# Kernel tuning notes

Measured on AMD Instinct MI355X. Metric: run time of the kernel, lower is better.

## Reference

```python
import jax, jax.numpy as jnp
import numpy as np

B, SL = 16, 512
S = SL - 1            # context length after shift (length=1)
E = 256               # embedding_size / hidden_size
NH = 4                # num_heads
K = 4                 # conv1d_kernel_size
I = 2 * E             # mLSTM inner dim (_inner_embedding_dim = 2*E)
DHM = I // NH         # mLSTM head dim
DHS = E // NH         # sLSTM head dim
NB, BS = I // 4, 4    # qkv_proj_blocksize=4 block-diagonal projections
F = 384               # gated FFN up dim = round_up(1.3*256, 64)
NUM_SKILLS, NUM_Q = 500, 10000
EPS = 1e-5


def _ln(x, w):
    mu = x.mean(-1, keepdims=True)
    var = x.var(-1, keepdims=True)
    return (x - mu) / jnp.sqrt(var + EPS) * w


def _causal_dwconv(x, w, b):
    # x: (B,S,C), depthwise causal conv with kernel (C,K)
    xt = jnp.transpose(x, (0, 2, 1))
    y = jax.lax.conv_general_dilated(
        xt, w[:, None, :], (1,), [(K - 1, 0)],
        dimension_numbers=('NCH', 'OIH', 'NCH'),
        feature_group_count=x.shape[-1])
    return jnp.transpose(y, (0, 2, 1)) + b


def _headwise(x, w):
    # block-diagonal linear: w (NB, BS, BS)
    xb = x.reshape(x.shape[0], x.shape[1], NB, BS)
    return jnp.einsum('bsnd,nod->bsno', xb, w).reshape(x.shape)


def _forward(questions, responses, skills,
             q_embed, qa_embed, q_embed_diff, qa_embed_diff, difficult_param,
             ln0_w, m_up_w, m_up_b, m_conv_w, m_conv_b, m_q_w, m_k_w, m_v_w,
             m_ig_w, m_ig_b, m_fg_w, m_fg_b, m_outnorm_w, m_skip, m_down_w, m_down_b,
             ln1_w, s_conv_w, s_conv_b, s_gate_w, s_rec_w, s_bias, s_gn_w,
             ln2_w, ffn_up_w, ffn_up_b, ffn_down_w, ffn_down_b,
             postnorm_w, out_w1, out_b1, out_w2, out_b2, out_w3, out_b3):
    pid = questions[:, :-1]
    q_data = skills[:, :-1]
    q_shft = skills[:, 1:]
    target = (responses * (responses > -1).astype(responses.dtype))[:, :-1]

    q_e = q_embed[q_data]                              # (B,S,E)
    qa_e = qa_embed[target] + q_e
    pid_e = difficult_param[pid]                       # (B,S,1)
    q_e = q_e + pid_e * q_embed_diff[q_data]
    qa_e = qa_e + pid_e * qa_embed_diff[target]

    # ---- xLSTM stack: block 0 = mLSTM block, block 1 = sLSTM block + gated FFN ----
    x = qa_e  # dropout is identity in eval

    # mLSTM block: x = x + mlstm_layer(LN(x))
    h = _ln(x, ln0_w)
    up = h @ m_up_w.T + m_up_b                         # (B,S,2I)
    x_m, z = jnp.split(up, 2, axis=-1)
    xc = jax.nn.silu(_causal_dwconv(x_m, m_conv_w, m_conv_b))
    q = _headwise(xc, m_q_w)
    k = _headwise(xc, m_k_w)
    v = _headwise(x_m, m_v_w)
    ifin = jnp.concatenate([q, k, v], axis=-1)         # (B,S,3I)
    ig = jnp.einsum('bsf,hf->bhs', ifin, m_ig_w) + m_ig_b[None, :, None]
    fg = jnp.einsum('bsf,hf->bhs', ifin, m_fg_w) + m_fg_b[None, :, None]
    qh = q.reshape(B, S, NH, DHM).transpose(0, 2, 1, 3)
    kh = k.reshape(B, S, NH, DHM).transpose(0, 2, 1, 3)
    vh = v.reshape(B, S, NH, DHM).transpose(0, 2, 1, 3)
    # parallel stabilized mLSTM
    logf = jax.nn.log_sigmoid(fg)                      # (B,NH,S)
    cs = jnp.concatenate([jnp.zeros((B, NH, 1), logf.dtype), jnp.cumsum(logf, -1)], -1)
    dmat = cs[:, :, 1:, None] - cs[:, :, None, 1:]     # (B,NH,S,S): sum of logf over (s,t]
    ltr = jnp.tril(jnp.ones((S, S), bool))
    logD = jnp.where(ltr, dmat, -jnp.inf) + ig[:, :, None, :]
    maxD = jnp.max(logD, -1, keepdims=True)
    D = jnp.exp(logD - maxD)
    qk = jnp.einsum('bhtd,bhsd->bhts', qh, kh) * (DHM ** -0.5)
    C = qk * D
    norm = jnp.maximum(jnp.abs(C.sum(-1, keepdims=True)), jnp.exp(-maxD))
    hh = jnp.einsum('bhts,bhsd->bhtd', C / (norm + 1e-6), vh)
    # multi-head layernorm (per head over DHM), weight on flattened dim
    hn = (hh - hh.mean(-1, keepdims=True)) / jnp.sqrt(hh.var(-1, keepdims=True) + EPS)
    hflat = hn.transpose(0, 2, 1, 3).reshape(B, S, I) * m_outnorm_w
    hout = (hflat + m_skip * xc) * jax.nn.silu(z)
    x = x + (hout @ m_down_w.T + m_down_b)

    # sLSTM block: x = x + slstm_layer(LN(x)); x = x + ffn(LN(x))
    h = _ln(x, ln1_w)
    hc = jax.nn.silu(_causal_dwconv(h, s_conv_w, s_conv_b))
    hh4 = h.reshape(B, S, NH, DHS)
    hc4 = hc.reshape(B, S, NH, DHS)
    gi = jnp.einsum('bsnd,nod->bsno', hc4, s_gate_w[0])   # i,f from conv path
    gf = jnp.einsum('bsnd,nod->bsno', hc4, s_gate_w[1])
    gz = jnp.einsum('bsnd,nod->bsno', hh4, s_gate_w[2])   # z,o from x path
    go = jnp.einsum('bsnd,nod->bsno', hh4, s_gate_w[3])
    wx = jnp.stack([gi, gf, gz, go], axis=2) + s_bias[None, None]  # (B,S,4,NH,DHS)

    def step(carry, wx_t):
        y, c, n, m = carry
        raw = wx_t + jnp.einsum('bnd,gnde->bgne', y, s_rec_w)
        iraw, fraw, zraw, oraw = raw[:, 0], raw[:, 1], raw[:, 2], raw[:, 3]
        logfplusm = m + jax.nn.log_sigmoid(fraw)
        mnew = jnp.maximum(iraw, logfplusm)
        ig_ = jnp.exp(iraw - mnew)
        fg_ = jnp.exp(logfplusm - mnew)
        cnew = fg_ * c + ig_ * jnp.tanh(zraw)
        nnew = fg_ * n + ig_
        ynew = jax.nn.sigmoid(oraw) * cnew / nnew
        return (ynew, cnew, nnew, mnew), ynew

    z0 = jnp.zeros((B, NH, DHS), x.dtype)
    _, ys = jax.lax.scan(step, (z0, z0, z0, z0), jnp.swapaxes(wx, 0, 1))
    y = jnp.swapaxes(ys, 0, 1)                           # (B,S,NH,DHS)
    yn = (y - y.mean(-1, keepdims=True)) / jnp.sqrt(y.var(-1, keepdims=True) + EPS)
    x = x + yn.reshape(B, S, E) * s_gn_w

    # gated FFN (relu)
    h = _ln(x, ln2_w)
    gate, upf = jnp.split(h @ ffn_up_w.T + ffn_up_b, 2, axis=-1)
    x = x + (jax.nn.relu(gate) * upf) @ ffn_down_w.T + ffn_down_b

    d = _ln(x, postnorm_w)                               # post_blocks_norm

    fam = jnp.where((target == 1)[..., None], d, 0.0)
    unfam = jnp.where((target == 0)[..., None], d, 0.0)
    d2 = d - pid_e
    cq = jnp.concatenate([d2, q_e, fam, unfam], axis=-1)  # (B,S,4E)
    o = jax.nn.relu(cq @ out_w1.T + out_b1)
    o = jax.nn.relu(o @ out_w2.T + out_b2)
    probs = jax.nn.sigmoid(o @ out_w3.T + out_b3)
    pred = jnp.take_along_axis(probs, q_shft[..., None], axis=-1)[..., 0]
    return pred                                          # (B,S)


def setup_inputs():
    key = jax.random.key(0)
    ks = iter(jax.random.split(key, 64))
    def rn(shape, s=0.02):
        return jax.random.normal(next(ks), shape, jnp.float32) * s
    return dict(
        questions=jax.random.randint(next(ks), (B, SL), 0, NUM_Q),
        responses=jax.random.randint(next(ks), (B, SL), 0, 2),
        skills=jax.random.randint(next(ks), (B, SL), 0, NUM_SKILLS),
        attention_mask=jnp.ones((B, SL), jnp.int32),
        q_embed=rn((NUM_SKILLS, E), 1.0),
        qa_embed=rn((2, E), 1.0),
        q_embed_diff=rn((NUM_SKILLS + 1, E), 1.0),
        qa_embed_diff=rn((2 * NUM_SKILLS + 1, E), 1.0),
        difficult_param=rn((NUM_Q + 1, 1), 0.1),
        ln0_w=jnp.ones((E,)),
        m_up_w=rn((2 * I, E)), m_up_b=jnp.zeros((2 * I,)),
        m_conv_w=rn((I, K), 0.1), m_conv_b=jnp.zeros((I,)),
        m_q_w=rn((NB, BS, BS), 0.1), m_k_w=rn((NB, BS, BS), 0.1), m_v_w=rn((NB, BS, BS), 0.1),
        m_ig_w=rn((NH, 3 * I)), m_ig_b=jnp.zeros((NH,)),
        m_fg_w=rn((NH, 3 * I)), m_fg_b=jnp.zeros((NH,)),
        m_outnorm_w=jnp.ones((I,)), m_skip=jnp.ones((I,)),
        m_down_w=rn((E, I)), m_down_b=jnp.zeros((E,)),
        ln1_w=jnp.ones((E,)),
        s_conv_w=rn((E, K), 0.1), s_conv_b=jnp.zeros((E,)),
        s_gate_w=rn((4, NH, DHS, DHS), 0.1),
        s_rec_w=rn((4, NH, DHS, DHS), 0.05),
        s_bias=jnp.zeros((4, NH, DHS)),
        s_gn_w=jnp.ones((E,)),
        ln2_w=jnp.ones((E,)),
        ffn_up_w=rn((2 * F, E)), ffn_up_b=jnp.zeros((2 * F,)),
        ffn_down_w=rn((E, F)), ffn_down_b=jnp.zeros((E,)),
        postnorm_w=jnp.ones((E,)),
        out_w1=rn((2 * E, 4 * E)), out_b1=jnp.zeros((2 * E,)),
        out_w2=rn((E, 2 * E)), out_b2=jnp.zeros((E,)),
        out_w3=rn((NUM_SKILLS, E)), out_b3=jnp.zeros((NUM_SKILLS,)),
    )


def reference(questions, responses, skills, attention_mask,
              q_embed, qa_embed, q_embed_diff, qa_embed_diff, difficult_param,
              ln0_w, m_up_w, m_up_b, m_conv_w, m_conv_b, m_q_w, m_k_w, m_v_w,
              m_ig_w, m_ig_b, m_fg_w, m_fg_b, m_outnorm_w, m_skip, m_down_w, m_down_b,
              ln1_w, s_conv_w, s_conv_b, s_gate_w, s_rec_w, s_bias, s_gn_w,
              ln2_w, ffn_up_w, ffn_up_b, ffn_down_w, ffn_down_b,
              postnorm_w, out_w1, out_b1, out_w2, out_b2, out_w3, out_b3):
    return _forward(questions, responses, skills,
                    q_embed, qa_embed, q_embed_diff, qa_embed_diff, difficult_param,
                    ln0_w, m_up_w, m_up_b, m_conv_w, m_conv_b, m_q_w, m_k_w, m_v_w,
                    m_ig_w, m_ig_b, m_fg_w, m_fg_b, m_outnorm_w, m_skip, m_down_w, m_down_b,
                    ln1_w, s_conv_w, s_conv_b, s_gate_w, s_rec_w, s_bias, s_gn_w,
                    ln2_w, ffn_up_w, ffn_up_b, ffn_down_w, ffn_down_b,
                    postnorm_w, out_w1, out_b1, out_w2, out_b2, out_w3, out_b3)
```

## Files before the change

kernel.cpp:

```cpp
#include <hip/hip_runtime.h>
#include <hip/hip_bf16.h>

#define B_    16
#define SL_   512
#define S_    511
#define E_    256
#define NH_   4
#define I_    512
#define DHM_  128
#define DHS_  64
#define F_    384
#define NP_   8192
#define NROW  (B_*S_)
#define EPS_  1e-5f

typedef __hip_bfloat16 bf16;
typedef unsigned short u16;
typedef __bf16 bf16x8v __attribute__((ext_vector_type(8)));
typedef float  f32x4v  __attribute__((ext_vector_type(4)));

__device__ __forceinline__ float rcp_(float x){ return __builtin_amdgcn_rcpf(x); }
__device__ __forceinline__ float sig_(float x){ return rcp_(1.f+__expf(-x)); }
__device__ __forceinline__ float silu_(float x){ return x*sig_(x); }
__device__ __forceinline__ float logsig_(float x){ return fminf(x,0.f) - __logf(1.f + __expf(-fabsf(x))); }
__device__ __forceinline__ float expneg_(float x){ return __expf(fminf(x,0.f)); }
__device__ __forceinline__ float expclamp_(float x){ return __expf(fminf(fmaxf(x,-80.f),80.f)); }
__device__ __forceinline__ float tanh_(float x){ return 1.f - 2.f*rcp_(__expf(2.f*x)+1.f); }

__global__ __launch_bounds__(256) void k_cvt16(const float* __restrict__ src, bf16* __restrict__ dst, int n){
  int i=blockIdx.x*256+threadIdx.x;
  if(i<n) dst[i]=__float2bfloat16(src[i]);
}
__global__ __launch_bounds__(256) void k_cvt16i(const float* __restrict__ src, bf16* __restrict__ dst){
  int i=blockIdx.x*256+threadIdx.x;
  int rp=i>>8, c=i&255;
  int j=rp>>1, p=rp&1;
  dst[i]=__float2bfloat16(src[(size_t)(j + p*F_)*E_ + c]);
}
__global__ __launch_bounds__(256) void k_cvtsplit(const float* __restrict__ src,
  bf16* __restrict__ hi, bf16* __restrict__ lo, int n){
  int i=blockIdx.x*256+threadIdx.x;
  if(i<n){
    float v=src[i];
    bf16 h=__float2bfloat16(v);
    hi[i]=h;
    lo[i]=__float2bfloat16(v-__bfloat162float(h));
  }
}
__global__ __launch_bounds__(256) void k_wtrans(const float* __restrict__ src, float* __restrict__ dst){
  int i = blockIdx.x*256+threadIdx.x;
  int blk = i>>12;
  int d = (i>>6)&63;
  int e = i&63;
  dst[(size_t)(blk*64+d)*64+e] = src[(size_t)(blk*64+e)*64+d];
}

__global__ __launch_bounds__(256) void k_wfrag(const float* __restrict__ rw, bf16* __restrict__ wf){
  int i = blockIdx.x*256+threadIdx.x;
  int j  = i&7;
  int l  = (i>>3)&63;
  int kf = (i>>9)&1;
  int t  = (i>>10)&15;
  int n  = i>>14;
  int g = t>>2;
  int e = (t&3)*16 + (l&15);
  int d = (l>>4)*16 + kf*8 + j;
  wf[i] = __float2bfloat16(rw[((size_t)((g*4+n)*64 + d))*64 + e]);
}

__global__ __launch_bounds__(256) void k_embed(
  const int* __restrict__ questions, const int* __restrict__ responses, const int* __restrict__ skills,
  const float* __restrict__ q_embed, const float* __restrict__ qa_embed,
  const float* __restrict__ q_embed_diff, const float* __restrict__ qa_embed_diff,
  const float* __restrict__ difficult_param, const float* __restrict__ ln0w,
  float* __restrict__ x, float* __restrict__ qe,
  bf16* __restrict__ h_hi, bf16* __restrict__ h_lo,
  float* __restrict__ pide, int* __restrict__ tgt, int* __restrict__ qsh)
{
  __shared__ float red[256];
  int r = blockIdx.x; int e = threadIdx.x;
  float xa = 0.f;
  if (r < NROW){
    int b = r / S_, s = r % S_;
    int pid  = questions[b*SL_+s];
    int qd   = skills[b*SL_+s];
    int resp = responses[b*SL_+s];
    int t    = (resp > -1) ? resp : 0;
    float pe = difficult_param[pid];
    float q0 = q_embed[qd*E_+e];
    xa = q0 + qa_embed[t*E_+e] + pe*qa_embed_diff[t*E_+e];
    float qn = q0 + pe*q_embed_diff[qd*E_+e];
    x[(size_t)r*E_+e]=xa; qe[(size_t)r*E_+e]=qn;
    if (e==0){ pide[r]=pe; tgt[r]=t; qsh[r]=skills[b*SL_+s+1]; }
  } else {
    x[(size_t)r*E_+e]=0.f; qe[(size_t)r*E_+e]=0.f;
    if (e==0){ pide[r]=0.f; tgt[r]=-7; qsh[r]=0; }
  }
  red[e]=xa; __syncthreads();
  for(int s2=128;s2>0;s2>>=1){ if(e<s2) red[e]+=red[e+s2]; __syncthreads(); }
  float mu = red[0]*(1.f/E_); __syncthreads();
  float d = xa-mu;
  red[e]=d*d; __syncthreads();
  for(int s2=128;s2>0;s2>>=1){ if(e<s2) red[e]+=red[e+s2]; __syncthreads(); }
  float var = red[0]*(1.f/E_);
  float o = d*rsqrtf(var+EPS_)*ln0w[e];
  bf16 hv = __float2bfloat16(o);
  h_hi[(size_t)r*E_+e] = hv;
  h_lo[(size_t)r*E_+e] = __float2bfloat16(o-__bfloat162float(hv));
}

__global__ __launch_bounds__(256) void k_ln(
  const float* __restrict__ in, const float* __restrict__ w, float* __restrict__ out)
{
  __shared__ float red[256];
  int r = blockIdx.x, t = threadIdx.x;
  float v = in[(size_t)r*E_+t];
  red[t]=v; __syncthreads();
  for(int s=128;s>0;s>>=1){ if(t<s) red[t]+=red[t+s]; __syncthreads(); }
  float mu = red[0]*(1.f/E_); __syncthreads();
  float d = v-mu;
  red[t]=d*d; __syncthreads();
  for(int s=128;s>0;s>>=1){ if(t<s) red[t]+=red[t+s]; __syncthreads(); }
  float var = red[0]*(1.f/E_);
  out[(size_t)r*E_+t] = d*rsqrtf(var+EPS_)*w[t];
}

__global__ __launch_bounds__(256) void k_gemm16s(
  const bf16* __restrict__ Ah, const bf16* __restrict__ Al,
  const bf16* __restrict__ Bh, const bf16* __restrict__ Bl,
  const float* __restrict__ bias, float* __restrict__ C, int M, int K)
{
  int tid=threadIdx.x;
  int wave=tid>>6, lane=tid&63;
  int wr=wave>>1, wc=wave&1;
  int row0=blockIdx.y*64 + wr*32;
  int col0=blockIdx.x*64 + wc*32;
  int lrow = lane&15, lq = lane>>4;
  f32x4v acc[2][2] = {};
  size_t aoff = (size_t)(row0+lrow)*K + lq*8;
  size_t boff = (size_t)(col0+lrow)*K + lq*8;
  for(int k0=0;k0<K;k0+=32){
    bf16x8v ah0=*(const bf16x8v*)(Ah+aoff+k0), ah1=*(const bf16x8v*)(Ah+aoff+(size_t)16*K+k0);
    bf16x8v al0=*(const bf16x8v*)(Al+aoff+k0), al1=*(const bf16x8v*)(Al+aoff+(size_t)16*K+k0);
    bf16x8v bh0=*(const bf16x8v*)(Bh+boff+k0), bh1=*(const bf16x8v*)(Bh+boff+(size_t)16*K+k0);
    bf16x8v bl0=*(const bf16x8v*)(Bl+boff+k0), bl1=*(const bf16x8v*)(Bl+boff+(size_t)16*K+k0);
    acc[0][0]=__builtin_amdgcn_mfma_f32_16x16x32_bf16(ah0,bh0,acc[0][0],0,0,0);
    acc[0][1]=__builtin_amdgcn_mfma_f32_16x16x32_bf16(ah0,bh1,acc[0][1],0,0,0);
    acc[1][0]=__builtin_amdgcn_mfma_f32_16x16x32_bf16(ah1,bh0,acc[1][0],0,0,0);
    acc[1][1]=__builtin_amdgcn_mfma_f32_16x16x32_bf16(ah1,bh1,acc[1][1],0,0,0);
    acc[0][0]=__builtin_amdgcn_mfma_f32_16x16x32_bf16(ah0,bl0,acc[0][0],0,0,0);
    acc[0][1]=__builtin_amdgcn_mfma_f32_16x16x32_bf16(ah0,bl1,acc[0][1],0,0,0);
    acc[1][0]=__builtin_amdgcn_mfma_f32_16x16x32_bf16(ah1,bl0,acc[1][0],0,0,0);
    acc[1][1]=__builtin_amdgcn_mfma_f32_16x16x32_bf16(ah1,bl1,acc[1][1],0,0,0);
    acc[0][0]=__builtin_amdgcn_mfma_f32_16x16x32_bf16(al0,bh0,acc[0][0],0,0,0);
    acc[0][1]=__builtin_amdgcn_mfma_f32_16x16x32_bf16(al0,bh1,acc[0][1],0,0,0);
    acc[1][0]=__builtin_amdgcn_mfma_f32_16x16x32_bf16(al1,bh0,acc[1][0],0,0,0);
    acc[1][1]=__builtin_amdgcn_mfma_f32_16x16x32_bf16(al1,bh1,acc[1][1],0,0,0);
  }
  #pragma unroll
  for(int mi=0;mi<2;mi++){
    #pragma unroll
    for(int ni=0;ni<2;ni++){
      #pragma unroll
      for(int r=0;r<4;r++){
        int row=row0+mi*16+lq*4+r;
        int col=col0+ni*16+lrow;
        C[(size_t)row*M+col]=acc[mi][ni][r] + bias[col];
      }
    }
  }
}

__global__ __launch_bounds__(256) void k_gemm16(
  const bf16* __restrict__ A, const bf16* __restrict__ Bw,
  const float* __restrict__ bias, const float* __restrict__ resid,
  float* __restrict__ C, bf16* __restrict__ C16,
  int M, int K, int relu)
{
  int tid=threadIdx.x;
  int wave=tid>>6, lane=tid&63;
  int wr=wave>>1, wc=wave&1;
  int row0=blockIdx.y*64 + wr*32;
  int col0=blockIdx.x*64 + wc*32;
  int lrow = lane&15, lq = lane>>4;
  f32x4v acc[2][2] = {};
  const bf16* Abase = A  + (size_t)(row0+lrow)*K + lq*8;
  const bf16* Bbase = Bw + (size_t)(col0+lrow)*K + lq*8;
  for(int k0=0;k0<K;k0+=32){
    bf16x8v a0 = *(const bf16x8v*)(Abase + k0);
    bf16x8v a1 = *(const bf16x8v*)(Abase + (size_t)16*K + k0);
    bf16x8v b0 = *(const bf16x8v*)(Bbase + k0);
    bf16x8v b1 = *(const bf16x8v*)(Bbase + (size_t)16*K + k0);
    acc[0][0]=__builtin_amdgcn_mfma_f32_16x16x32_bf16(a0,b0,acc[0][0],0,0,0);
    acc[0][1]=__builtin_amdgcn_mfma_f32_16x16x32_bf16(a0,b1,acc[0][1],0,0,0);
    acc[1][0]=__builtin_amdgcn_mfma_f32_16x16x32_bf16(a1,b0,acc[1][0],0,0,0);
    acc[1][1]=__builtin_amdgcn_mfma_f32_16x16x32_bf16(a1,b1,acc[1][1],0,0,0);
  }
  #pragma unroll
  for(int mi=0;mi<2;mi++){
    #pragma unroll
    for(int ni=0;ni<2;ni++){
      #pragma unroll
      for(int r=0;r<4;r++){
        int row=row0+mi*16+lq*4+r;
        int col=col0+ni*16+lrow;
        float v=acc[mi][ni][r] + (bias? bias[col]:0.f);
        if(relu) v=fmaxf(v,0.f);
        if(resid) v += resid[(size_t)row*M+col];
        if(C)   C[(size_t)row*M+col]=v;
        if(C16) C16[(size_t)row*M+col]=__float2bfloat16(v);
      }
    }
  }
}

__global__ __launch_bounds__(256) void k_gemm16f(
  const bf16* __restrict__ A, const bf16* __restrict__ Bw,
  const float* __restrict__ bias, bf16* __restrict__ out, int K)
{
  int tid=threadIdx.x;
  int wave=tid>>6, lane=tid&63;
  int wr=wave>>1, wc=wave&1;
  int row0=blockIdx.y*64 + wr*32;
  int col0=blockIdx.x*64 + wc*32;
  int lrow = lane&15, lq = lane>>4;
  f32x4v acc[2][2] = {};
  const bf16* Abase = A  + (size_t)(row0+lrow)*K + lq*8;
  const bf16* Bbase = Bw + (size_t)(col0+lrow)*K + lq*8;
  for(int k0=0;k0<K;k0+=32){
    bf16x8v a0 = *(const bf16x8v*)(Abase + k0);
    bf16x8v a1 = *(const bf16x8v*)(Abase + (size_t)16*K + k0);
    bf16x8v b0 = *(const bf16x8v*)(Bbase + k0);
    bf16x8v b1 = *(const bf16x8v*)(Bbase + (size_t)16*K + k0);
    acc[0][0]=__builtin_amdgcn_mfma_f32_16x16x32_bf16(a0,b0,acc[0][0],0,0,0);
    acc[0][1]=__builtin_amdgcn_mfma_f32_16x16x32_bf16(a0,b1,acc[0][1],0,0,0);
    acc[1][0]=__builtin_amdgcn_mfma_f32_16x16x32_bf16(a1,b0,acc[1][0],0,0,0);
    acc[1][1]=__builtin_amdgcn_mfma_f32_16x16x32_bf16(a1,b1,acc[1][1],0,0,0);
  }
  #pragma unroll
  for(int mi=0;mi<2;mi++){
    #pragma unroll
    for(int ni=0;ni<2;ni++){
      #pragma unroll
      for(int r=0;r<4;r++){
        int row=row0+mi*16+lq*4+r;
        int col=col0+ni*16+lrow;
        float v=acc[mi][ni][r] + bias[(col>>1) + (col&1)*F_];
        float o = __shfl_xor(v, 1, 64);
        if(!(lrow&1)){
          out[(size_t)row*F_ + (col>>1)] = __float2bfloat16(fmaxf(v,0.f)*o);
        }
      }
    }
  }
}

__global__ __launch_bounds__(256) void k_conv_silu(
  const float* __restrict__ in, int ild, const float* __restrict__ w, const float* __restrict__ bws,
  float* __restrict__ out, int old_, int C)
{
  int i = blockIdx.x*256 + threadIdx.x;
  int r = i / C, c = i % C;
  if (r >= NP_) return;
  float acc = 0.f;
  if (r < NROW) {
    int b=r/S_, s=r%S_;
    acc = bws[c];
    #pragma unroll
    for(int j=0;j<4;j++){
      int ss=s-3+j;
      if(ss>=0) acc += w[c*4+j] * in[(size_t)(b*S_+ss)*ild + c];
    }
    acc = silu_(acc);
  }
  out[(size_t)r*old_ + c] = acc;
}

__global__ __launch_bounds__(256) void k_headwise(
  const float* __restrict__ xc, const float* __restrict__ xm, int xmld,
  const float* __restrict__ wq, const float* __restrict__ wk, const float* __restrict__ wv,
  bf16* __restrict__ qhi, bf16* __restrict__ qlo,
  bf16* __restrict__ khi, bf16* __restrict__ klo,
  bf16* __restrict__ vhi, bf16* __restrict__ vlo)
{
  int i=blockIdx.x*256+threadIdx.x;
  int r=i/I_, c=i%I_;
  if(r>=NP_) return;
  size_t oi=(size_t)r*I_+c;
  if(r>=NROW){
    bf16 z=__float2bfloat16(0.f);
    qhi[oi]=z; qlo[oi]=z; khi[oi]=z; klo[oi]=z; vhi[oi]=z; vlo[oi]=z;
    return;
  }
  int n=c>>2, o=c&3;
  const float* xcr = xc + (size_t)r*I_ + n*4;
  const float* xmr = xm + (size_t)r*xmld + n*4;
  float aq=0.f, ak=0.f, av=0.f;
  #pragma unroll
  for(int d=0;d<4;d++){
    float xcv=xcr[d], xmv=xmr[d];
    aq += xcv*wq[(n*4+o)*4+d];
    ak += xcv*wk[(n*4+o)*4+d];
    av += xmv*wv[(n*4+o)*4+d];
  }
  bf16 qh=__float2bfloat16(aq); qhi[oi]=qh; qlo[oi]=__float2bfloat16(aq-__bfloat162float(qh));
  bf16 kh=__float2bfloat16(ak); khi[oi]=kh; klo[oi]=__float2bfloat16(ak-__bfloat162float(kh));
  bf16 vh=__float2bfloat16(av); vhi[oi]=vh; vlo[oi]=__float2bfloat16(av-__bfloat162float(vh));
}

__global__ __launch_bounds__(256) void k_igfg(
  const bf16* __restrict__ qhi, const bf16* __restrict__ qlo,
  const bf16* __restrict__ khi, const bf16* __restrict__ klo,
  const bf16* __restrict__ vhi, const bf16* __restrict__ vlo,
  const float* __restrict__ wig, const float* __restrict__ big,
  const float* __restrict__ wfg, const float* __restrict__ bfg,
  float* __restrict__ igb, float* __restrict__ fgb)
{
  int r=blockIdx.x;
  int h=threadIdx.x>>6, lane=threadIdx.x&63;
  int b=r/S_, s=r%S_;
  float acc_i=0.f, acc_f=0.f;
  for(int f=lane; f<1536; f+=64){
    float val;
    if (f<512)       val = __bfloat162float(qhi[(size_t)r*512+f])      + __bfloat162float(qlo[(size_t)r*512+f]);
    else if (f<1024) val = __bfloat162float(khi[(size_t)r*512+f-512])  + __bfloat162float(klo[(size_t)r*512+f-512]);
    else             val = __bfloat162float(vhi[(size_t)r*512+f-1024]) + __bfloat162float(vlo[(size_t)r*512+f-1024]);
    acc_i += val*wig[h*1536+f];
    acc_f += val*wfg[h*1536+f];
  }
  for(int m=32;m;m>>=1){ acc_i+=__shfl_xor(acc_i,m,64); acc_f+=__shfl_xor(acc_f,m,64); }
  if(lane==0){
    igb[(b*4+h)*512+s]=acc_i+big[h];
    fgb[(b*4+h)*512+s]=acc_f+bfg[h];
  }
}

__global__ __launch_bounds__(256) void k_decay(
  const float* __restrict__ igb, const float* __restrict__ fgb,
  float* __restrict__ cs1, float* __restrict__ g, float* __restrict__ M)
{
  int bh = blockIdx.x; int tid = threadIdx.x;
  __shared__ float buf[512];
  __shared__ float buf2[512];
  for (int s=tid; s<512; s+=256)
    buf[s] = (s<S_) ? logsig_(fgb[bh*512+s]) : 0.f;
  __syncthreads();
  for (int off=1; off<512; off<<=1){
    int s0=tid, s1=tid+256;
    float v0 = buf[s0] + ((s0>=off)? buf[s0-off] : 0.f);
    float v1 = buf[s1] + ((s1>=off)? buf[s1-off] : 0.f);
    __syncthreads();
    buf[s0]=v0; buf[s1]=v1;
    __syncthreads();
  }
  for (int s=tid; s<512; s+=256){
    float c = buf[s];
    if (s<S_){
      cs1[bh*512+s]=c;
      float gv = igb[bh*512+s]-c;
      g[bh*512+s]=gv;
      buf2[s]=gv;
    } else buf2[s] = -3.4e38f;
  }
  __syncthreads();
  for (int off=1; off<512; off<<=1){
    int s0=tid, s1=tid+256;
    float v0 = fmaxf(buf2[s0], (s0>=off)? buf2[s0-off] : -3.4e38f);
    float v1 = fmaxf(buf2[s1], (s1>=off)? buf2[s1-off] : -3.4e38f);
    __syncthreads();
    buf2[s0]=v0; buf2[s1]=v1;
    __syncthreads();
  }
  for (int s=tid; s<S_; s+=256) M[bh*512+s] = buf2[s];
}

#define TQ 32
#define TS 32
__global__ __launch_bounds__(256) void k_attn(
  const bf16* __restrict__ qhi, const bf16* __restrict__ qlo,
  const bf16* __restrict__ khi, const bf16* __restrict__ klo,
  const bf16* __restrict__ vhi, const bf16* __restrict__ vlo,
  const float* __restrict__ cs1, const float* __restrict__ g, const float* __restrict__ M,
  const float* __restrict__ onw, const float* __restrict__ skip,
  const float* __restrict__ xc, const float* __restrict__ zA,
  bf16* __restrict__ out16)
{
  __shared__ __align__(16) u16 vThi[128][40];
  __shared__ __align__(16) u16 vTlo[128][40];
  __shared__ __align__(16) u16 phi[32][40];
  __shared__ __align__(16) u16 plo[32][40];
  __shared__ float MtS[32], cssS[32], normS[32], muS[32], rsS[32];
  __shared__ float lsumW[2][32], sumA[2][32], sumB[2][32];

  int tq = blockIdx.x, bh = blockIdx.y;
  int b = bh>>2, h = bh&3;
  int tid = threadIdx.x;
  int wv = tid>>6;
  int tw = wv&1, sw = wv>>1;
  int l = tid&63;
  int lr = l&15, lg = l>>4;
  int t0 = tq*TQ;
  const float sc = 0.08838834764831843f;

  if (tid < 32){
    int t = t0 + tid; int tc = (t<S_)? t : (S_-1);
    MtS[tid]  = M[bh*512 + tc];
    cssS[tid] = cs1[bh*512 + tc];
  }

  bf16x8v qh[4], ql[4];
  {
    size_t qoff = ((size_t)(b*S_ + t0 + tw*16 + lr))*512 + h*128 + lg*8;
    #pragma unroll
    for(int k0=0;k0<4;k0++){
      qh[k0] = *(const bf16x8v*)(qhi + qoff + k0*32);
      ql[k0] = *(const bf16x8v*)(qlo + qoff + k0*32);
    }
  }

  f32x4v accpv[4] = {};
  float lsum[4] = {0.f,0.f,0.f,0.f};

  int t1 = min(t0+TQ, S_);
  int sp = tid>>4, dl = tid&15;

  __syncthreads();

  for (int s0=0; s0<t1; s0+=TS){
    bf16x8v kh[4], kl2[4];
    {
      size_t koff = ((size_t)(b*S_ + s0 + sw*16 + lr))*512 + h*128 + lg*8;
      #pragma unroll
      for(int k0=0;k0<4;k0++){
        kh[k0]  = *(const bf16x8v*)(khi + koff + k0*32);
        kl2[k0] = *(const bf16x8v*)(klo + koff + k0*32);
      }
    }
    u16 vha[8], vhb[8], vla[8], vlb[8];
    {
      const u16* ha = (const u16*)vhi + ((size_t)(b*S_ + s0 + 2*sp))*512 + h*128 + dl;
      const u16* la = (const u16*)vlo + ((size_t)(b*S_ + s0 + 2*sp))*512 + h*128 + dl;
      #pragma unroll
      for(int j=0;j<8;j++){
        vha[j]=ha[16*j]; vhb[j]=ha[512+16*j];
        vla[j]=la[16*j]; vlb[j]=la[512+16*j];
      }
    }
    float g_s = g[bh*512 + s0 + sw*16 + lr];

    f32x4v cqk = {0.f,0.f,0.f,0.f};
    #pragma unroll
    for(int k0=0;k0<4;k0++){
      cqk = __builtin_amdgcn_mfma_f32_16x16x32_bf16(qh[k0], kh[k0],  cqk, 0,0,0);
      cqk = __builtin_amdgcn_mfma_f32_16x16x32_bf16(qh[k0], kl2[k0], cqk, 0,0,0);
      cqk = __builtin_amdgcn_mfma_f32_16x16x32_bf16(ql[k0], kh[k0],  cqk, 0,0,0);
    }

    int s_g = s0 + sw*16 + lr;
    u16 pw_h[4], pw_l[4];
    #pragma unroll
    for(int r=0;r<4;r++){
      int tl = tw*16 + lg*4 + r;
      int t_row = t0 + tl;
      float wvv = ((s_g <= t_row) && (t_row < S_)) ? cqk[r]*sc*expneg_(g_s - MtS[tl]) : 0.f;
      lsum[r] += wvv;
      bf16 hh = __float2bfloat16(wvv);
      float hf = __bfloat162float(hh);
      bf16 ll = __float2bfloat16(wvv - hf);
      __builtin_memcpy(&pw_h[r], &hh, 2);
      __builtin_memcpy(&pw_l[r], &ll, 2);
    }

    __syncthreads();

    #pragma unroll
    for(int r=0;r<4;r++){
      int tl = tw*16 + lg*4 + r;
      phi[tl][sw*16 + lr] = pw_h[r];
      plo[tl][sw*16 + lr] = pw_l[r];
    }
    {
      unsigned* vh32 = (unsigned*)&vThi[0][0];
      unsigned* vl32 = (unsigned*)&vTlo[0][0];
      #pragma unroll
      for(int j=0;j<8;j++){
        int d = dl + 16*j;
        vh32[d*20 + sp] = (unsigned)vha[j] | ((unsigned)vhb[j]<<16);
        vl32[d*20 + sp] = (unsigned)vla[j] | ((unsigned)vlb[j]<<16);
      }
    }

    __syncthreads();

    bf16x8v pah = *(const bf16x8v*)((const void*)(&phi[tw*16 + lr][0] + lg*8));
    bf16x8v pal = *(const bf16x8v*)((const void*)(&plo[tw*16 + lr][0] + lg*8));
    #pragma unroll
    for(int fd=0; fd<4; fd++){
      bf16x8v vbh = *(const bf16x8v*)((const void*)(&vThi[sw*64 + fd*16 + lr][0] + lg*8));
      bf16x8v vbl = *(const bf16x8v*)((const void*)(&vTlo[sw*64 + fd*16 + lr][0] + lg*8));
      accpv[fd] = __builtin_amdgcn_mfma_f32_16x16x32_bf16(pah, vbh, accpv[fd], 0,0,0);
      accpv[fd] = __builtin_amdgcn_mfma_f32_16x16x32_bf16(pah, vbl, accpv[fd], 0,0,0);
      accpv[fd] = __builtin_amdgcn_mfma_f32_16x16x32_bf16(pal, vbh, accpv[fd], 0,0,0);
    }
  }

  #pragma unroll
  for(int r=0;r<4;r++){
    #pragma unroll
    for(int m=1;m<16;m<<=1) lsum[r] += __shfl_xor(lsum[r], m, 16);
  }
  if (lr==0){
    #pragma unroll
    for(int r=0;r<4;r++) lsumW[sw][tw*16 + lg*4 + r] = lsum[r];
  }
  __syncthreads();
  if (tid < 32){
    float ls = lsumW[0][tid] + lsumW[1][tid];
    float maxD = cssS[tid] + MtS[tid];
    float nrm = fmaxf(fabsf(ls), expclamp_(-maxD));
    normS[tid] = rcp_(nrm + 1e-6f);
  }
  __syncthreads();

  float o_[4][4];
  float srow[4]={0.f,0.f,0.f,0.f}, sq[4]={0.f,0.f,0.f,0.f};
  #pragma unroll
  for(int r=0;r<4;r++){
    float scl = normS[tw*16 + lg*4 + r];
    #pragma unroll
    for(int fd=0;fd<4;fd++){
      float o = accpv[fd][r]*scl;
      o_[fd][r] = o;
      srow[r] += o; sq[r] += o*o;
    }
  }
  #pragma unroll
  for(int r=0;r<4;r++){
    #pragma unroll
    for(int m=1;m<16;m<<=1){ srow[r]+=__shfl_xor(srow[r],m,16); sq[r]+=__shfl_xor(sq[r],m,16); }
  }
  if (lr==0){
    #pragma unroll
    for(int r=0;r<4;r++){ sumA[sw][tw*16+lg*4+r]=srow[r]; sumB[sw][tw*16+lg*4+r]=sq[r]; }
  }
  __syncthreads();
  if (tid < 32){
    float mu = (sumA[0][tid]+sumA[1][tid])*(1.f/128.f);
    float ex2= (sumB[0][tid]+sumB[1][tid])*(1.f/128.f);
    muS[tid]=mu;
    rsS[tid]=rsqrtf(fmaxf(ex2 - mu*mu, 0.f)+EPS_);
  }
  __syncthreads();

  #pragma unroll
  for(int fd=0; fd<4; fd++){
    int d = sw*64 + fd*16 + lr;
    float ow = onw[h*128 + d];
    float sk = skip[h*128 + d];
    #pragma unroll
    for(int r=0;r<4;r++){
      int tl = tw*16 + lg*4 + r;
      int t = t0 + tl;
      if (t < S_){
        size_t row = (size_t)(b*S_+t);
        float hf = (o_[fd][r]-muS[tl])*rsS[tl]*ow;
        float xcv = xc[row*512 + h*128 + d];
        float zv  = zA[row*1024 + 512 + h*128 + d];
        out16[row*512 + h*128 + d] = __float2bfloat16((hf + sk*xcv)*silu_(zv));
      }
    }
  }
}

#define WXR 64
__global__ __launch_bounds__(256,2) void k_wx(
  const float* __restrict__ h, const float* __restrict__ hc,
  const float* __restrict__ gwT, const float* __restrict__ gb,
  float* __restrict__ wx)
{
  int rt = blockIdx.x, g = blockIdx.y;
  int tid = threadIdx.x;
  int n = tid>>6, e = tid&63;
  const float* src = (g<2)? hc : h;
  __shared__ __align__(16) float hs[WXR][260];
  float W[64];
  #pragma unroll
  for(int d=0;d<64;d++) W[d] = gwT[(size_t)(((g*4+n)*64+d))*64 + e];
  float bias = gb[(g*4+n)*64+e];
  int row0 = rt*WXR;
  for(int idx=tid; idx<WXR*64; idx+=256){
    int rr = idx>>6, cc4 = (idx&63)*4;
    *(float4*)&hs[rr][cc4] = *(const float4*)(src + (size_t)(row0+rr)*256 + cc4);
  }
  __syncthreads();
  #pragma unroll 4
  for(int rr=0; rr<WXR; ++rr){
    int r = row0+rr;
    if (r>=NROW) break;
    const float* hrow = &hs[rr][n*64];
    float a0=0,a1=0,a2=0,a3=0;
    #pragma unroll
    for(int d=0;d<64;d+=4){
      float4 hv = *(const float4*)&hrow[d];
      a0+=hv.x*W[d]; a1+=hv.y*W[d+1]; a2+=hv.z*W[d+2]; a3+=hv.w*W[d+3];
    }
    int b=r/S_, s=r%S_;
    wx[(((size_t)(b*4+n)*512 + s)*256) + e*4 + g] = bias + ((a0+a1)+(a2+a3));
  }
}

__global__ __launch_bounds__(256,1) void k_scan(
  const float* __restrict__ wx, const bf16* __restrict__ wf, float* __restrict__ y_out)
{
  int bn = blockIdx.x; int b = bn>>2, n = bn&3;
  int tid = threadIdx.x;
  int w = tid>>6;
  int l = tid&63;
  int q = l>>4;
  int el = l&15;
  int e  = w*16 + el;

  __shared__ __align__(16) unsigned short ybuf[2][64];

  if (tid < 128) ((unsigned short*)ybuf)[tid] = 0;
  __syncthreads();

  bf16x8v Wf2[4][2];
  #pragma unroll
  for(int g=0; g<4; ++g){
    #pragma unroll
    for(int kf=0; kf<2; ++kf){
      Wf2[g][kf] = *(const bf16x8v*)(wf + ((size_t)((n*16 + (4*g+w))*2 + kf)*64 + l)*8);
    }
  }

  const float* wxBase = wx + ((size_t)bn*512)*256 + e*4;
  float* yst = y_out + (size_t)(b*S_)*256 + n*64 + e;

  float4 p0,p1,p2,p3;
  p0 = *(const float4*)(wxBase + (size_t)0*256);
  p1 = *(const float4*)(wxBase + (size_t)1*256);
  p2 = *(const float4*)(wxBase + (size_t)2*256);
  p3 = *(const float4*)(wxBase + (size_t)3*256);

  f32x4v z4 = {0.f,0.f,0.f,0.f};
  float c=0.f, nn=0.f, pm=1.f;

  for (int s=0; s<S_; ++s){
    int p = s&1;
    bf16x8v a0 = *(const bf16x8v*)&ybuf[p][16*q];
    bf16x8v a1 = *(const bf16x8v*)&ybuf[p][16*q+8];

    f32x4v acc0,acc1,acc2,acc3, accb0,accb1,accb2,accb3;
    acc0  = __builtin_amdgcn_mfma_f32_16x16x32_bf16(a0, Wf2[0][0], z4, 0,0,0);
    acc1  = __builtin_amdgcn_mfma_f32_16x16x32_bf16(a0, Wf2[1][0], z4, 0,0,0);
    acc2  = __builtin_amdgcn_mfma_f32_16x16x32_bf16(a0, Wf2[2][0], z4, 0,0,0);
    acc3  = __builtin_amdgcn_mfma_f32_16x16x32_bf16(a0, Wf2[3][0], z4, 0,0,0);
    accb0 = __builtin_amdgcn_mfma_f32_16x16x32_bf16(a1, Wf2[0][1], z4, 0,0,0);
    accb1 = __builtin_amdgcn_mfma_f32_16x16x32_bf16(a1, Wf2[1][1], z4, 0,0,0);
    accb2 = __builtin_amdgcn_mfma_f32_16x16x32_bf16(a1, Wf2[2][1], z4, 0,0,0);
    accb3 = __builtin_amdgcn_mfma_f32_16x16x32_bf16(a1, Wf2[3][1], z4, 0,0,0);

    float4 wg = p0; p0=p1; p1=p2; p2=p3;
    { int sp = s+4; if (sp>510) sp=510;
      p3 = *(const float4*)(wxBase + (size_t)sp*256); }

    float iraw=acc0[0]+accb0[0]+wg.x, fraw=acc1[0]+accb1[0]+wg.y;
    float zraw=acc2[0]+accb2[0]+wg.z, oraw=acc3[0]+accb3[0]+wg.w;

    float pe  = __expf(fminf(iraw, 80.f));
    float ef  = __expf(-fraw);
    float e2z = __expf(2.f*zraw);
    float eo  = __expf(-oraw);
    float sf  = rcp_(1.f+ef);
    float ps  = pm*sf;
    float pn  = fmaxf(fmaxf(pe, ps), 1e-30f);
    float rpn = rcp_(pn);
    float fg  = ps*rpn;
    float ig  = pe*rpn;
    float th  = 1.f - 2.f*rcp_(e2z+1.f);
    c  = fg*c + ig*th;
    nn = fmaxf(fg*nn + ig, 1e-30f);
    float y = rcp_(1.f+eo) * c * rcp_(nn);
    pm = pn;

    bf16 hb = __float2bfloat16(y);
    unsigned short hbits; __builtin_memcpy(&hbits,&hb,2);
    if (l < 16){
      ybuf[p^1][e] = hbits;
      yst[(size_t)s*256] = y;
    }
    asm volatile("s_waitcnt lgkmcnt(0)" ::: "memory");
    __builtin_amdgcn_s_barrier();
    asm volatile("" ::: "memory");
    __builtin_amdgcn_sched_barrier(0);
  }
}

__global__ __launch_bounds__(256) void k_ynadd_ln2(
  const float* __restrict__ y, const float* __restrict__ gn,
  float* __restrict__ x, const float* __restrict__ ln2w, bf16* __restrict__ h16)
{
  __shared__ float red[256];
  int r=blockIdx.x, t=threadIdx.x;
  float xv = x[(size_t)r*256+t];
  if (r < NROW){
    float v=y[(size_t)r*256+t];
    float s=v;
    for(int m=32;m;m>>=1) s+=__shfl_xor(s,m,64);
    float mu=s*(1.f/64.f);
    float d=v-mu;
    float q=d*d;
    for(int m=32;m;m>>=1) q+=__shfl_xor(q,m,64);
    float var=q*(1.f/64.f);
    xv += d*rsqrtf(var+EPS_)*gn[t];
    x[(size_t)r*256+t]=xv;
  }
  red[t]=xv; __syncthreads();
  for(int s=128;s>0;s>>=1){ if(t<s) red[t]+=red[t+s]; __syncthreads(); }
  float mu2=red[0]*(1.f/E_); __syncthreads();
  float dd=xv-mu2;
  red[t]=dd*dd; __syncthreads();
  for(int s=128;s>0;s>>=1){ if(t<s) red[t]+=red[t+s]; __syncthreads(); }
  float var2=red[0]*(1.f/E_);
  h16[(size_t)r*256+t]=__float2bfloat16(dd*rsqrtf(var2+EPS_)*ln2w[t]);
}

__global__ __launch_bounds__(256) void k_cq_ln(
  const float* __restrict__ x, const float* __restrict__ pw,
  const float* __restrict__ qe, const float* __restrict__ pide, const int* __restrict__ tgt,
  bf16* __restrict__ cq)
{
  __shared__ float red[256];
  int r=blockIdx.x, t=threadIdx.x;
  float v = x[(size_t)r*256+t];
  red[t]=v; __syncthreads();
  for(int s=128;s>0;s>>=1){ if(t<s) red[t]+=red[t+s]; __syncthreads(); }
  float mu=red[0]*(1.f/E_); __syncthreads();
  float d=v-mu;
  red[t]=d*d; __syncthreads();
  for(int s=128;s>0;s>>=1){ if(t<s) red[t]+=red[t+s]; __syncthreads(); }
  float var=red[0]*(1.f/E_);
  float dv = d*rsqrtf(var+EPS_)*pw[t];
  float pe=pide[r]; int tg=tgt[r];
  size_t base=(size_t)r*1024;
  cq[base+t]=__float2bfloat16(dv-pe);
  cq[base+256+t]=__float2bfloat16(qe[(size_t)r*256+t]);
  cq[base+512+t]=__float2bfloat16((tg==1)? dv:0.f);
  cq[base+768+t]=__float2bfloat16((tg==0)? dv:0.f);
}

__global__ __launch_bounds__(256) void k_final(
  const float* __restrict__ o2, const float* __restrict__ w3, const float* __restrict__ b3,
  const int* __restrict__ qsh, float* __restrict__ out)
{
  __shared__ float red[256];
  int r=blockIdx.x, t=threadIdx.x;
  int qi=qsh[r];
  float p=o2[(size_t)r*256+t]*w3[(size_t)qi*256+t];
  red[t]=p; __syncthreads();
  for(int s=128;s>0;s>>=1){ if(t<s) red[t]+=red[t+s]; __syncthreads(); }
  if(t==0) out[r]=sig_(red[0]+b3[qi]);
}

extern "C" void kernel_launch(void* const* d_in, const int* in_sizes, int n_in,
                              void* d_out, int out_size, void* d_ws, size_t ws_size,
                              hipStream_t stream) {
  const int* questions = (const int*)d_in[0];
  const int* responses = (const int*)d_in[1];
  const int* skills    = (const int*)d_in[2];
  const float* q_embed       = (const float*)d_in[4];
  const float* qa_embed      = (const float*)d_in[5];
  const float* q_embed_diff  = (const float*)d_in[6];
  const float* qa_embed_diff = (const float*)d_in[7];
  const float* difficult_param=(const float*)d_in[8];
  const float* ln0_w   = (const float*)d_in[9];
  const float* m_up_w  = (const float*)d_in[10];
  const float* m_up_b  = (const float*)d_in[11];
  const float* m_conv_w= (const float*)d_in[12];
  const float* m_conv_b= (const float*)d_in[13];
  const float* m_q_w   = (const float*)d_in[14];
  const float* m_k_w   = (const float*)d_in[15];
  const float* m_v_w   = (const float*)d_in[16];
  const float* m_ig_w  = (const float*)d_in[17];
  const float* m_ig_b  = (const float*)d_in[18];
  const float* m_fg_w  = (const float*)d_in[19];
  const float* m_fg_b  = (const float*)d_in[20];
  const float* m_outnorm_w=(const float*)d_in[21];
  const float* m_skip  = (const float*)d_in[22];
  const float* m_down_w= (const float*)d_in[23];
  const float* m_down_b= (const float*)d_in[24];
  const float* ln1_w   = (const float*)d_in[25];
  const float* s_conv_w= (const float*)d_in[26];
  const float* s_conv_b= (const float*)d_in[27];
  const float* s_gate_w= (const float*)d_in[28];
  const float* s_rec_w = (const float*)d_in[29];
  const float* s_bias  = (const float*)d_in[30];
  const float* s_gn_w  = (const float*)d_in[31];
  const float* ln2_w   = (const float*)d_in[32];
  const float* ffn_up_w= (const float*)d_in[33];
  const float* ffn_up_b= (const float*)d_in[34];
  const float* ffn_down_w=(const float*)d_in[35];
  const float* ffn_down_b=(const float*)d_in[36];
  const float* postnorm_w=(const float*)d_in[37];
  const float* out_w1  = (const float*)d_in[38];
  const float* out_b1  = (const float*)d_in[39];
  const float* out_w2  = (const float*)d_in[40];
  const float* out_b2  = (const float*)d_in[41];
  const float* out_w3  = (const float*)d_in[42];
  const float* out_b3  = (const float*)d_in[43];

  float* ws = (float*)d_ws;
  const size_t R = (size_t)NP_*256;
  float* x    = ws;
  float* qe   = ws + R;
  float* h    = ws + 2*R;
  float* t256 = ws + 3*R;
  float* A    = ws + 4*R;
  float* Bb   = ws + 8*R;
  float* Cb   = ws + 10*R;
  float* Db   = ws + 12*R;
  float* Eb   = ws + 14*R;
  float* pide = ws + 16*R;
  int*   tgt  = (int*)(ws + 16*R + NP_);
  int*   qsh  = (int*)(ws + 16*R + 2*NP_);
  float* igb  = ws + 16*R + 3*NP_;
  float* fgb  = igb + 64*512;
  float* cs1  = fgb + 64*512;
  float* gdec = cs1 + 64*512;
  float* Mrun = gdec + 64*512;
  bf16* wpool = (bf16*)(Mrun + 64*512);
  bf16* m_down_w16  = wpool;
  bf16* ffn_up_w16  = m_down_w16 + 256*512;
  bf16* ffn_down_w16= ffn_up_w16 + 768*256;
  bf16* out_w1_16   = ffn_down_w16 + 256*384;
  bf16* out_w2_16   = out_w1_16 + 512*1024;
  bf16* h16         = out_w2_16 + 256*512;
  bf16* m_up_whi    = h16 + (size_t)NP_*256;
  bf16* m_up_wlo    = m_up_whi + 1024*256;
  float* gwT        = (float*)(m_up_wlo + 1024*256);
  bf16* wfrag       = (bf16*)(gwT + 16*64*64);
  bf16* q_hi = (bf16*)Cb;  bf16* q_lo = q_hi + (size_t)NP_*512;
  bf16* k_hi = (bf16*)Db;  bf16* k_lo = k_hi + (size_t)NP_*512;
  bf16* v_hi = (bf16*)Eb;  bf16* v_lo = v_hi + (size_t)NP_*512;
  bf16* hout16 = (bf16*)h;
  bf16* ffg16  = (bf16*)Db;
  bf16* cq16   = (bf16*)Eb;
  bf16* b16    = (bf16*)Cb;
  bf16* h_hi   = (bf16*)t256;
  bf16* h_lo   = h_hi + (size_t)NP_*256;

  k_cvt16<<<(256*512+255)/256,256,0,stream>>>(m_down_w,  m_down_w16,  256*512);
  k_cvt16i<<<(768*256)/256,256,0,stream>>>(ffn_up_w, ffn_up_w16);
  k_cvt16<<<(256*384+255)/256,256,0,stream>>>(ffn_down_w,ffn_down_w16,256*384);
  k_cvt16<<<(512*1024+255)/256,256,0,stream>>>(out_w1,   out_w1_16,   512*1024);
  k_cvt16<<<(256*512+255)/256,256,0,stream>>>(out_w2,    out_w2_16,   256*512);
  k_cvtsplit<<<(1024*256+255)/256,256,0,stream>>>(m_up_w, m_up_whi, m_up_wlo, 1024*256);
  k_wtrans<<<(16*64*64)/256,256,0,stream>>>(s_gate_w, gwT);
  k_wfrag<<<65536/256,256,0,stream>>>(s_rec_w, wfrag);

  k_embed<<<NP_,256,0,stream>>>(questions,responses,skills,q_embed,qa_embed,
      q_embed_diff,qa_embed_diff,difficult_param, ln0_w, x,qe, h_hi,h_lo, pide,tgt,qsh);
  k_gemm16s<<<dim3(1024/64,NP_/64),256,0,stream>>>(h_hi,h_lo, m_up_whi,m_up_wlo, m_up_b, A, 1024,256);
  k_conv_silu<<<(NP_*512)/256,256,0,stream>>>(A,1024, m_conv_w,m_conv_b, Bb,512,512);
  k_headwise<<<(NP_*512)/256,256,0,stream>>>(Bb, A,1024, m_q_w,m_k_w,m_v_w,
      q_hi,q_lo, k_hi,k_lo, v_hi,v_lo);
  k_igfg<<<NROW,256,0,stream>>>(q_hi,q_lo, k_hi,k_lo, v_hi,v_lo, m_ig_w,m_ig_b,m_fg_w,m_fg_b, igb,fgb);
  k_decay<<<64,256,0,stream>>>(igb,fgb, cs1,gdec,Mrun);
  hipMemsetAsync(hout16 + (size_t)NROW*512, 0, (size_t)(NP_-NROW)*512*sizeof(bf16), stream);
  k_attn<<<dim3((S_+TQ-1)/TQ, B_*NH_),256,0,stream>>>(q_hi,q_lo, k_hi,k_lo, v_hi,v_lo,
      cs1,gdec,Mrun, m_outnorm_w, m_skip, Bb, A, hout16);
  k_gemm16<<<dim3(256/64,NP_/64),256,0,stream>>>(hout16, m_down_w16, m_down_b, x, x, (bf16*)nullptr, 256,512,0);
  k_ln<<<NP_,256,0,stream>>>(x, ln1_w, h);
  k_conv_silu<<<(NP_*256)/256,256,0,stream>>>(h,256, s_conv_w,s_conv_b, Bb,256,256);
  k_wx<<<dim3(128,4),256,0,stream>>>(h, Bb, gwT, s_bias, A);
  k_scan<<<64,256,0,stream>>>(A, wfrag, Cb);
  k_ynadd_ln2<<<NP_,256,0,stream>>>(Cb, s_gn_w, x, ln2_w, h16);
  k_gemm16f<<<dim3(768/64,NP_/64),256,0,stream>>>(h16, ffn_up_w16, ffn_up_b, ffg16, 256);
  k_gemm16<<<dim3(256/64,NP_/64),256,0,stream>>>(ffg16, ffn_down_w16, ffn_down_b, x, x, (bf16*)nullptr, 256,384,0);
  k_cq_ln<<<NP_,256,0,stream>>>(x, postnorm_w, qe, pide, tgt, cq16);
  k_gemm16<<<dim3(512/64,NP_/64),256,0,stream>>>(cq16, out_w1_16, out_b1, (const float*)nullptr, (float*)nullptr, b16, 512,1024,1);
  k_gemm16<<<dim3(256/64,NP_/64),256,0,stream>>>(b16, out_w2_16, out_b2, (const float*)nullptr, t256, (bf16*)nullptr, 256,512,1);
  k_final<<<NROW,256,0,stream>>>(t256, out_w3, out_b3, qsh, (float*)d_out);
}
```

Measured before the change: 839.5 us.

## Fuse weight-prep kernels and fuse conv/headwise/gate projections into one kernel

The eight weight conversion and transposition kernels are merged into a single k_prep launch that dispatches on a flat index. The causal conv+SiLU, block-diagonal q/k/v projection and input/forget gate reductions are fused into one per-row kernel, k_mega, which keeps intermediates in shared memory. This removes launch overhead and avoids re-reading the q/k/v hi/lo bf16 buffers and the conv output from global memory. The gate reduction now uses the fp32 q/k/v values rather than the hi+lo reconstruction, which slightly changes the numerics. The one-row-per-block layout also leaves the conv reads of neighbouring rows uncoalesced across blocks.

```diff
diff --git a/kernel.cpp b/kernel.cpp
--- a/kernel.cpp
+++ b/kernel.cpp
@@ -27,45 +27,50 @@
 __device__ __forceinline__ float expclamp_(float x){ return __expf(fminf(fmaxf(x,-80.f),80.f)); }
 __device__ __forceinline__ float tanh_(float x){ return 1.f - 2.f*rcp_(__expf(2.f*x)+1.f); }
 
-__global__ __launch_bounds__(256) void k_cvt16(const float* __restrict__ src, bf16* __restrict__ dst, int n){
-  int i=blockIdx.x*256+threadIdx.x;
-  if(i<n) dst[i]=__float2bfloat16(src[i]);
-}
-__global__ __launch_bounds__(256) void k_cvt16i(const float* __restrict__ src, bf16* __restrict__ dst){
-  int i=blockIdx.x*256+threadIdx.x;
-  int rp=i>>8, c=i&255;
-  int j=rp>>1, p=rp&1;
-  dst[i]=__float2bfloat16(src[(size_t)(j + p*F_)*E_ + c]);
-}
-__global__ __launch_bounds__(256) void k_cvtsplit(const float* __restrict__ src,
-  bf16* __restrict__ hi, bf16* __restrict__ lo, int n){
-  int i=blockIdx.x*256+threadIdx.x;
-  if(i<n){
-    float v=src[i];
-    bf16 h=__float2bfloat16(v);
-    hi[i]=h;
-    lo[i]=__float2bfloat16(v-__bfloat162float(h));
-  }
-}
-__global__ __launch_bounds__(256) void k_wtrans(const float* __restrict__ src, float* __restrict__ dst){
-  int i = blockIdx.x*256+threadIdx.x;
-  int blk = i>>12;
-  int d = (i>>6)&63;
-  int e = i&63;
-  dst[(size_t)(blk*64+d)*64+e] = src[(size_t)(blk*64+e)*64+d];
-}
-
-__global__ __launch_bounds__(256) void k_wfrag(const float* __restrict__ rw, bf16* __restrict__ wf){
-  int i = blockIdx.x*256+threadIdx.x;
-  int j  = i&7;
-  int l  = (i>>3)&63;
-  int kf = (i>>9)&1;
-  int t  = (i>>10)&15;
-  int n  = i>>14;
-  int g = t>>2;
-  int e = (t&3)*16 + (l&15);
-  int d = (l>>4)*16 + kf*8 + j;
-  wf[i] = __float2bfloat16(rw[((size_t)((g*4+n)*64 + d))*64 + e]);
+__global__ __launch_bounds__(256) void k_prep(
+  const float* __restrict__ m_down_w, bf16* __restrict__ m_down_w16,
+  const float* __restrict__ ffn_up_w, bf16* __restrict__ ffn_up_w16,
+  const float* __restrict__ ffn_down_w, bf16* __restrict__ ffn_down_w16,
+  const float* __restrict__ out_w1, bf16* __restrict__ out_w1_16,
+  const float* __restrict__ out_w2, bf16* __restrict__ out_w2_16,
+  const float* __restrict__ m_up_w, bf16* __restrict__ m_up_whi, bf16* __restrict__ m_up_wlo,
+  const float* __restrict__ s_gate_w, float* __restrict__ gwT,
+  const float* __restrict__ s_rec_w, bf16* __restrict__ wfrag)
+{
+  int i = blockIdx.x*256 + threadIdx.x;
+  if (i < 131072){ m_down_w16[i] = __float2bfloat16(m_down_w[i]); return; }
+  i -= 131072;
+  if (i < 196608){
+    int rp=i>>8, c=i&255; int j=rp>>1, p=rp&1;
+    ffn_up_w16[i] = __float2bfloat16(ffn_up_w[(size_t)(j + p*F_)*E_ + c]); return;
+  }
+  i -= 196608;
+  if (i < 98304){ ffn_down_w16[i] = __float2bfloat16(ffn_down_w[i]); return; }
+  i -= 98304;
+  if (i < 524288){ out_w1_16[i] = __float2bfloat16(out_w1[i]); return; }
+  i -= 524288;
+  if (i < 131072){ out_w2_16[i] = __float2bfloat16(out_w2[i]); return; }
+  i -= 131072;
+  if (i < 262144){
+    float v = m_up_w[i];
+    bf16 h = __float2bfloat16(v);
+    m_up_whi[i]=h;
+    m_up_wlo[i]=__float2bfloat16(v-__bfloat162float(h));
+    return;
+  }
+  i -= 262144;
+  if (i < 65536){
+    int blk=i>>12, d=(i>>6)&63, e=i&63;
+    gwT[(size_t)(blk*64+d)*64+e] = s_gate_w[(size_t)(blk*64+e)*64+d]; return;
+  }
+  i -= 65536;
+  {
+    int j=i&7, l=(i>>3)&63, kf=(i>>9)&1, t=(i>>10)&15, n=i>>14;
+    int g=t>>2;
+    int e=(t&3)*16 + (l&15);
+    int d=(l>>4)*16 + kf*8 + j;
+    wfrag[i] = __float2bfloat16(s_rec_w[((size_t)((g*4+n)*64 + d))*64 + e]);
+  }
 }
 
 __global__ __launch_bounds__(256) void k_embed(
@@ -276,62 +281,73 @@
   out[(size_t)r*old_ + c] = acc;
 }
 
-__global__ __launch_bounds__(256) void k_headwise(
-  const float* __restrict__ xc, const float* __restrict__ xm, int xmld,
+__global__ __launch_bounds__(256) void k_mega(
+  const float* __restrict__ A,
+  const float* __restrict__ cw, const float* __restrict__ cb,
   const float* __restrict__ wq, const float* __restrict__ wk, const float* __restrict__ wv,
+  const float* __restrict__ wig, const float* __restrict__ big,
+  const float* __restrict__ wfg, const float* __restrict__ bfg,
+  float* __restrict__ xcout,
   bf16* __restrict__ qhi, bf16* __restrict__ qlo,
   bf16* __restrict__ khi, bf16* __restrict__ klo,
-  bf16* __restrict__ vhi, bf16* __restrict__ vlo)
-{
-  int i=blockIdx.x*256+threadIdx.x;
-  int r=i/I_, c=i%I_;
-  if(r>=NP_) return;
-  size_t oi=(size_t)r*I_+c;
-  if(r>=NROW){
-    bf16 z=__float2bfloat16(0.f);
-    qhi[oi]=z; qlo[oi]=z; khi[oi]=z; klo[oi]=z; vhi[oi]=z; vlo[oi]=z;
+  bf16* __restrict__ vhi, bf16* __restrict__ vlo,
+  float* __restrict__ igb, float* __restrict__ fgb)
+{
+  __shared__ float xcs[512];
+  __shared__ float xms[512];
+  __shared__ float qs[512], ks[512], vs[512];
+  int r = blockIdx.x;
+  int tid = threadIdx.x;
+  if (r >= NROW){
+    bf16 z = __float2bfloat16(0.f);
+    size_t o = (size_t)r*512 + tid*2;
+    qhi[o]=z; qhi[o+1]=z; qlo[o]=z; qlo[o+1]=z;
+    khi[o]=z; khi[o+1]=z; klo[o]=z; klo[o+1]=z;
+    vhi[o]=z; vhi[o+1]=z; vlo[o]=z; vlo[o+1]=z;
     return;
   }
-  int n=c>>2, o=c&3;
-  const float* xcr = xc + (size_t)r*I_ + n*4;
-  const float* xmr = xm + (size_t)r*xmld + n*4;
-  float aq=0.f, ak=0.f, av=0.f;
-  #pragma unroll
-  for(int d=0;d<4;d++){
-    float xcv=xcr[d], xmv=xmr[d];
-    aq += xcv*wq[(n*4+o)*4+d];
-    ak += xcv*wk[(n*4+o)*4+d];
-    av += xmv*wv[(n*4+o)*4+d];
-  }
-  bf16 qh=__float2bfloat16(aq); qhi[oi]=qh; qlo[oi]=__float2bfloat16(aq-__bfloat162float(qh));
-  bf16 kh=__float2bfloat16(ak); khi[oi]=kh; klo[oi]=__float2bfloat16(ak-__bfloat162float(kh));
-  bf16 vh=__float2bfloat16(av); vhi[oi]=vh; vlo[oi]=__float2bfloat16(av-__bfloat162float(vh));
-}
-
-__global__ __launch_bounds__(256) void k_igfg(
-  const bf16* __restrict__ qhi, const bf16* __restrict__ qlo,
-  const bf16* __restrict__ khi, const bf16* __restrict__ klo,
-  const bf16* __restrict__ vhi, const bf16* __restrict__ vlo,
-  const float* __restrict__ wig, const float* __restrict__ big,
-  const float* __restrict__ wfg, const float* __restrict__ bfg,
-  float* __restrict__ igb, float* __restrict__ fgb)
-{
-  int r=blockIdx.x;
-  int h=threadIdx.x>>6, lane=threadIdx.x&63;
   int b=r/S_, s=r%S_;
-  float acc_i=0.f, acc_f=0.f;
+  const float* arow = A + (size_t)r*1024;
+  for (int c=tid; c<512; c+=256){
+    float acc = cb[c];
+    #pragma unroll
+    for(int j=0;j<4;j++){
+      int ss=s-3+j;
+      if(ss>=0) acc += cw[c*4+j]*A[((size_t)(b*S_+ss))*1024 + c];
+    }
+    acc = silu_(acc);
+    xcs[c]=acc;
+    xcout[(size_t)r*512+c]=acc;
+    xms[c]=arow[c];
+  }
+  __syncthreads();
+  for (int c=tid; c<512; c+=256){
+    int n=c>>2, o=c&3;
+    float aq=0.f, ak=0.f, av=0.f;
+    #pragma unroll
+    for(int d=0;d<4;d++){
+      aq += xcs[n*4+d]*wq[(n*4+o)*4+d];
+      ak += xcs[n*4+d]*wk[(n*4+o)*4+d];
+      av += xms[n*4+d]*wv[(n*4+o)*4+d];
+    }
+    qs[c]=aq; ks[c]=ak; vs[c]=av;
+    size_t oi=(size_t)r*512+c;
+    bf16 qh=__float2bfloat16(aq); qhi[oi]=qh; qlo[oi]=__float2bfloat16(aq-__bfloat162float(qh));
+    bf16 kh=__float2bfloat16(ak); khi[oi]=kh; klo[oi]=__float2bfloat16(ak-__bfloat162float(kh));
+    bf16 vh=__float2bfloat16(av); vhi[oi]=vh; vlo[oi]=__float2bfloat16(av-__bfloat162float(vh));
+  }
+  __syncthreads();
+  int h = tid>>6, lane = tid&63;
+  float ai=0.f, af=0.f;
   for(int f=lane; f<1536; f+=64){
-    float val;
-    if (f<512)       val = __bfloat162float(qhi[(size_t)r*512+f])      + __bfloat162float(qlo[(size_t)r*512+f]);
-    else if (f<1024) val = __bfloat162float(khi[(size_t)r*512+f-512])  + __bfloat162float(klo[(size_t)r*512+f-512]);
-    else             val = __bfloat162float(vhi[(size_t)r*512+f-1024]) + __bfloat162float(vlo[(size_t)r*512+f-1024]);
-    acc_i += val*wig[h*1536+f];
-    acc_f += val*wfg[h*1536+f];
-  }
-  for(int m=32;m;m>>=1){ acc_i+=__shfl_xor(acc_i,m,64); acc_f+=__shfl_xor(acc_f,m,64); }
+    float val = (f<512)? qs[f] : (f<1024)? ks[f-512] : vs[f-1024];
+    ai += val*wig[h*1536+f];
+    af += val*wfg[h*1536+f];
+  }
+  for(int m=32;m;m>>=1){ ai+=__shfl_xor(ai,m,64); af+=__shfl_xor(af,m,64); }
   if(lane==0){
-    igb[(b*4+h)*512+s]=acc_i+big[h];
-    fgb[(b*4+h)*512+s]=acc_f+bfg[h];
+    igb[(b*4+h)*512+s]=ai+big[h];
+    fgb[(b*4+h)*512+s]=af+bfg[h];
   }
 }
 
@@ -850,22 +866,16 @@
   bf16* h_hi   = (bf16*)t256;
   bf16* h_lo   = h_hi + (size_t)NP_*256;
 
-  k_cvt16<<<(256*512+255)/256,256,0,stream>>>(m_down_w,  m_down_w16,  256*512);
-  k_cvt16i<<<(768*256)/256,256,0,stream>>>(ffn_up_w, ffn_up_w16);
-  k_cvt16<<<(256*384+255)/256,256,0,stream>>>(ffn_down_w,ffn_down_w16,256*384);
-  k_cvt16<<<(512*1024+255)/256,256,0,stream>>>(out_w1,   out_w1_16,   512*1024);
-  k_cvt16<<<(256*512+255)/256,256,0,stream>>>(out_w2,    out_w2_16,   256*512);
-  k_cvtsplit<<<(1024*256+255)/256,256,0,stream>>>(m_up_w, m_up_whi, m_up_wlo, 1024*256);
-  k_wtrans<<<(16*64*64)/256,256,0,stream>>>(s_gate_w, gwT);
-  k_wfrag<<<65536/256,256,0,stream>>>(s_rec_w, wfrag);
+  k_prep<<<5760,256,0,stream>>>(
+      m_down_w, m_down_w16, ffn_up_w, ffn_up_w16, ffn_down_w, ffn_down_w16,
+      out_w1, out_w1_16, out_w2, out_w2_16, m_up_w, m_up_whi, m_up_wlo,
+      s_gate_w, gwT, s_rec_w, wfrag);
 
   k_embed<<<NP_,256,0,stream>>>(questions,responses,skills,q_embed,qa_embed,
       q_embed_diff,qa_embed_diff,difficult_param, ln0_w, x,qe, h_hi,h_lo, pide,tgt,qsh);
   k_gemm16s<<<dim3(1024/64,NP_/64),256,0,stream>>>(h_hi,h_lo, m_up_whi,m_up_wlo, m_up_b, A, 1024,256);
-  k_conv_silu<<<(NP_*512)/256,256,0,stream>>>(A,1024, m_conv_w,m_conv_b, Bb,512,512);
-  k_headwise<<<(NP_*512)/256,256,0,stream>>>(Bb, A,1024, m_q_w,m_k_w,m_v_w,
-      q_hi,q_lo, k_hi,k_lo, v_hi,v_lo);
-  k_igfg<<<NROW,256,0,stream>>>(q_hi,q_lo, k_hi,k_lo, v_hi,v_lo, m_ig_w,m_ig_b,m_fg_w,m_fg_b, igb,fgb);
+  k_mega<<<NP_,256,0,stream>>>(A, m_conv_w,m_conv_b, m_q_w,m_k_w,m_v_w,
+      m_ig_w,m_ig_b,m_fg_w,m_fg_b, Bb, q_hi,q_lo, k_hi,k_lo, v_hi,v_lo, igb,fgb);
   k_decay<<<64,256,0,stream>>>(igb,fgb, cs1,gdec,Mrun);
   hipMemsetAsync(hout16 + (size_t)NROW*512, 0, (size_t)(NP_-NROW)*512*sizeof(bf16), stream);
   k_attn<<<dim3((S_+TQ-1)/TQ, B_*NH_),256,0,stream>>>(q_hi,q_lo, k_hi,k_lo, v_hi,v_lo,
```

Measured after the change: 800.4 us. -4.7%, faster.
